# Kernel optimization log

Measured on AMD Instinct MI355X. Metric: run time of the kernel, lower is better.

## Reference

```python
import jax, jax.numpy as jnp
import numpy as np

IN_CH = 256
OUT_CH = 256
NUM_HEADS = 8
N = 4096


def setup_inputs() -> dict:
    key = jax.random.key(0)
    ks = jax.random.split(key, 12)
    s = 0.02
    return {
        "vertex_features": jax.random.normal(ks[0], (N, IN_CH), dtype=jnp.float32),
        "relative_encoding": jax.random.normal(ks[1], (N, N, NUM_HEADS), dtype=jnp.float32),
        "num_nodes": N,
        "Wq": jax.random.normal(ks[2], (IN_CH, OUT_CH), dtype=jnp.float32) * s,
        "bq": jnp.zeros((OUT_CH,), dtype=jnp.float32),
        "Wk": jax.random.normal(ks[3], (IN_CH, OUT_CH), dtype=jnp.float32) * s,
        "bk": jnp.zeros((OUT_CH,), dtype=jnp.float32),
        "Wv": jax.random.normal(ks[4], (IN_CH, OUT_CH), dtype=jnp.float32) * s,
        "bv": jnp.zeros((OUT_CH,), dtype=jnp.float32),
        "W1": jax.random.normal(ks[5], (OUT_CH // NUM_HEADS, OUT_CH), dtype=jnp.float32) * s,
        "b1": jnp.zeros((OUT_CH,), dtype=jnp.float32),
        "W2": jax.random.normal(ks[6], (OUT_CH, OUT_CH), dtype=jnp.float32) * s,
        "b2": jnp.zeros((OUT_CH,), dtype=jnp.float32),
    }


def reference(vertex_features, relative_encoding, num_nodes, Wq, bq, Wk, bk, Wv, bv, W1, b1, W2, b2):
    H = relative_encoding.shape[-1]
    # torch view(N, d, H): channel axis splits as (d, heads)
    q = (vertex_features @ Wq + bq).reshape(num_nodes, -1, H)  # [N, d, H]
    k = (vertex_features @ Wk + bk).reshape(num_nodes, -1, H)  # [N, d, H]
    v = (vertex_features @ Wv + bv).reshape(num_nodes, -1, H)  # [N, d, H]
    # q.permute(2,0,1) @ k.permute(2,1,0) -> [H,N,N], then permute(1,2,0) -> [N,N,H]
    scores = jnp.einsum('idh,jdh->ijh', q, k) + relative_encoding  # [N, N, H]
    # NOTE: softmax over the HEAD axis (dim=-1 of [N,N,H]), as in the original
    attn = jax.nn.softmax(scores, axis=-1)
    # [N,N,H] @ [N,H,d] (batched over first N) -> [N,N,d], then sum over dim=1 -> [N,d]
    attn_out = jnp.einsum('ijh,jhd->id', attn, jnp.swapaxes(v, 1, 2))  # [N, d]
    hidden = jax.nn.relu(attn_out @ W1 + b1)
    output = hidden @ W2 + b2  # [N, OUT_CH]
    return output, attn
```

## Files before the change

kernel.cpp:

```cpp
#include <hip/hip_runtime.h>

#define NN 4096
#define CH 256
#define NHEAD 8
#define DHEAD 32

typedef __attribute__((ext_vector_type(8))) short bf8_t;
typedef __attribute__((ext_vector_type(4))) float f4_t;

__device__ __forceinline__ unsigned short f2bf(float f) {
    unsigned int u = __float_as_uint(f);
    u += 0x7FFFu + ((u >> 16) & 1u);
    return (unsigned short)(u >> 16);
}

__global__ __launch_bounds__(256) void qkv_kernel(
    const float* __restrict__ X,
    const float* __restrict__ Wq, const float* __restrict__ bq,
    const float* __restrict__ Wk, const float* __restrict__ bk,
    const float* __restrict__ Wv, const float* __restrict__ bv,
    unsigned short* __restrict__ Qbf, unsigned short* __restrict__ Kbf,
    unsigned short* __restrict__ Vbf, float* __restrict__ ao)
{
    __shared__ __align__(16) float xs[16 * 256];
    const int c = threadIdx.x;
    const int i0 = blockIdx.x * 16;
    for (int r = 0; r < 16; ++r) xs[r * 256 + c] = X[(size_t)(i0 + r) * 256 + c];
    ao[(size_t)i0 * 32 + c] = 0.f;
    ao[(size_t)i0 * 32 + 256 + c] = 0.f;
    __syncthreads();

    float aq[16], ak[16], av[16];
#pragma unroll
    for (int r = 0; r < 16; ++r) { aq[r] = 0.f; ak[r] = 0.f; av[r] = 0.f; }

    for (int k = 0; k < 256; k += 4) {
        float wq0 = Wq[(k + 0) * 256 + c], wq1 = Wq[(k + 1) * 256 + c];
        float wq2 = Wq[(k + 2) * 256 + c], wq3 = Wq[(k + 3) * 256 + c];
        float wk0 = Wk[(k + 0) * 256 + c], wk1 = Wk[(k + 1) * 256 + c];
        float wk2 = Wk[(k + 2) * 256 + c], wk3 = Wk[(k + 3) * 256 + c];
        float wv0 = Wv[(k + 0) * 256 + c], wv1 = Wv[(k + 1) * 256 + c];
        float wv2 = Wv[(k + 2) * 256 + c], wv3 = Wv[(k + 3) * 256 + c];
#pragma unroll
        for (int r = 0; r < 16; ++r) {
            const float4 x = *(const float4*)&xs[r * 256 + k];
            aq[r] += x.x * wq0 + x.y * wq1 + x.z * wq2 + x.w * wq3;
            ak[r] += x.x * wk0 + x.y * wk1 + x.z * wk2 + x.w * wk3;
            av[r] += x.x * wv0 + x.y * wv1 + x.z * wv2 + x.w * wv3;
        }
    }

    const int cs = (c & 7) * 32 + (c >> 3);
    const float bqv = bq[c], bkv = bk[c], bvv = bv[c];
#pragma unroll
    for (int r = 0; r < 16; ++r) {
        const size_t row = (size_t)(i0 + r) * 256;
        Qbf[row + cs] = f2bf(aq[r] + bqv);
        Kbf[row + cs] = f2bf(ak[r] + bkv);
        Vbf[row + c]  = f2bf(av[r] + bvv);
    }
}

__global__ __launch_bounds__(256) void attn_kernel(
    const unsigned short* __restrict__ Qbf, const unsigned short* __restrict__ Kbf,
    const unsigned short* __restrict__ Vbf, const float* __restrict__ rel,
    float* __restrict__ attn_g, float* __restrict__ ao)
{
    __shared__ __align__(16) float sc_s[2048];
    __shared__ __align__(16) unsigned short at_s[16 * 136];

    const int tid = threadIdx.x;
    const int w = tid >> 6, lane = tid & 63;
    const int quad = lane >> 4, l16 = lane & 15;
    const int i0 = blockIdx.x * 16;
    const int jbase = blockIdx.y * 1024;

    bf8_t qf[2];
#pragma unroll
    for (int e = 0; e < 2; ++e) {
        const int h = 2 * w + e;
        qf[e] = *(const bf8_t*)(Qbf + (size_t)(i0 + l16) * 256 + h * 32 + quad * 8);
    }

    f4_t pv0 = {0.f, 0.f, 0.f, 0.f};
    f4_t pv1 = {0.f, 0.f, 0.f, 0.f};

    const int so  = tid * 8;
    const int sri = so >> 7, src = so & 127;
    const int jlw = w * 4 + quad;
    const int smi = tid >> 4, smj = tid & 15;

    for (int jc = 0; jc < 64; ++jc) {
        const int jb = jbase + jc * 16;

        {
            const float* gp = rel + (size_t)(i0 + sri) * 32768 + (size_t)jb * 8 + src;
            const float4 v0 = *(const float4*)gp;
            const float4 v1 = *(const float4*)(gp + 4);
            *(float4*)&sc_s[so]     = v0;
            *(float4*)&sc_s[so + 4] = v1;
        }
        __syncthreads();

#pragma unroll
        for (int e = 0; e < 2; ++e) {
            const int h = 2 * w + e;
            const bf8_t kf = *(const bf8_t*)(Kbf + (size_t)(jb + l16) * 256 + h * 32 + quad * 8);
            f4_t cf;
#pragma unroll
            for (int r = 0; r < 4; ++r) cf[r] = sc_s[(quad * 4 + r) * 128 + l16 * 8 + h];
            const f4_t d = __builtin_amdgcn_mfma_f32_16x16x32_bf16(qf[e], kf, cf, 0, 0, 0);
#pragma unroll
            for (int r = 0; r < 4; ++r) sc_s[(quad * 4 + r) * 128 + l16 * 8 + h] = d[r];
        }
        __syncthreads();

        {
            const float* sp = &sc_s[smi * 128 + smj * 8];
            const float4 s0 = *(const float4*)sp;
            const float4 s1 = *(const float4*)(sp + 4);
            float e0 = __expf(s0.x), e1 = __expf(s0.y), e2 = __expf(s0.z), e3 = __expf(s0.w);
            float e4 = __expf(s1.x), e5 = __expf(s1.y), e6 = __expf(s1.z), e7 = __expf(s1.w);
            const float inv = 1.0f / (e0 + e1 + e2 + e3 + e4 + e5 + e6 + e7);
            e0 *= inv; e1 *= inv; e2 *= inv; e3 *= inv;
            e4 *= inv; e5 *= inv; e6 *= inv; e7 *= inv;
            float* gp = attn_g + ((size_t)(i0 + smi) * 4096 + (size_t)(jb + smj)) * 8;
            *(float4*)gp       = make_float4(e0, e1, e2, e3);
            *(float4*)(gp + 4) = make_float4(e4, e5, e6, e7);
            const unsigned int p0 = (unsigned int)f2bf(e0) | ((unsigned int)f2bf(e1) << 16);
            const unsigned int p1 = (unsigned int)f2bf(e2) | ((unsigned int)f2bf(e3) << 16);
            const unsigned int p2 = (unsigned int)f2bf(e4) | ((unsigned int)f2bf(e5) << 16);
            const unsigned int p3 = (unsigned int)f2bf(e6) | ((unsigned int)f2bf(e7) << 16);
            *(uint4*)&at_s[smi * 136 + smj * 8] = make_uint4(p0, p1, p2, p3);
        }
        __syncthreads();

        {
            const bf8_t af = *(const bf8_t*)&at_s[l16 * 136 + jlw * 8];
            const unsigned short* vb = Vbf + (size_t)(jb + jlw) * 256;
            const bf8_t v0 = *(const bf8_t*)(vb + l16 * 8);
            const bf8_t v1 = *(const bf8_t*)(vb + 128 + l16 * 8);
            pv0 = __builtin_amdgcn_mfma_f32_16x16x32_bf16(af, v0, pv0, 0, 0, 0);
            pv1 = __builtin_amdgcn_mfma_f32_16x16x32_bf16(af, v1, pv1, 0, 0, 0);
        }
    }

#pragma unroll
    for (int r = 0; r < 4; ++r) {
        const size_t row = (size_t)(i0 + quad * 4 + r) * 32;
        atomicAdd(&ao[row + l16], pv0[r]);
        atomicAdd(&ao[row + 16 + l16], pv1[r]);
    }
}

__global__ __launch_bounds__(256) void mlp_kernel(
    const float* __restrict__ ao, const float* __restrict__ W1, const float* __restrict__ b1,
    const float* __restrict__ W2, const float* __restrict__ b2, float* __restrict__ out)
{
    __shared__ __align__(16) float aos[16 * 32];
    __shared__ __align__(16) float hid[16 * 256];
    const int c = threadIdx.x;
    const int i0 = blockIdx.x * 16;
    aos[c]       = ao[(size_t)i0 * 32 + c];
    aos[c + 256] = ao[(size_t)i0 * 32 + 256 + c];
    __syncthreads();

    float w1r[32];
#pragma unroll
    for (int d = 0; d < 32; ++d) w1r[d] = W1[d * 256 + c];
    const float b1v = b1[c];
    for (int r = 0; r < 16; ++r) {
        float h = b1v;
#pragma unroll
        for (int d = 0; d < 32; ++d) h += aos[r * 32 + d] * w1r[d];
        hid[r * 256 + c] = fmaxf(h, 0.f);
    }
    __syncthreads();

    float acc[16];
    const float b2v = b2[c];
#pragma unroll
    for (int r = 0; r < 16; ++r) acc[r] = b2v;
    for (int k = 0; k < 256; k += 4) {
        const float w20 = W2[(k + 0) * 256 + c], w21 = W2[(k + 1) * 256 + c];
        const float w22 = W2[(k + 2) * 256 + c], w23 = W2[(k + 3) * 256 + c];
#pragma unroll
        for (int r = 0; r < 16; ++r) {
            const float4 hh = *(const float4*)&hid[r * 256 + k];
            acc[r] += hh.x * w20 + hh.y * w21 + hh.z * w22 + hh.w * w23;
        }
    }
#pragma unroll
    for (int r = 0; r < 16; ++r) out[(size_t)(i0 + r) * 256 + c] = acc[r];
}

extern "C" void kernel_launch(void* const* d_in, const int* in_sizes, int n_in,
                              void* d_out, int out_size, void* d_ws, size_t ws_size,
                              hipStream_t stream)
{
    const float* X   = (const float*)d_in[0];
    const float* rel = (const float*)d_in[1];
    const float* Wq  = (const float*)d_in[3];
    const float* bq  = (const float*)d_in[4];
    const float* Wk  = (const float*)d_in[5];
    const float* bk  = (const float*)d_in[6];
    const float* Wv  = (const float*)d_in[7];
    const float* bv  = (const float*)d_in[8];
    const float* W1  = (const float*)d_in[9];
    const float* b1  = (const float*)d_in[10];
    const float* W2  = (const float*)d_in[11];
    const float* b2  = (const float*)d_in[12];

    float* out    = (float*)d_out;
    float* attn_g = out + (size_t)NN * CH;

    unsigned short* Qbf = (unsigned short*)d_ws;
    unsigned short* Kbf = Qbf + (size_t)NN * CH;
    unsigned short* Vbf = Kbf + (size_t)NN * CH;
    float* ao = (float*)(Vbf + (size_t)NN * CH);

    qkv_kernel<<<dim3(256), dim3(256), 0, stream>>>(X, Wq, bq, Wk, bk, Wv, bv, Qbf, Kbf, Vbf, ao);
    attn_kernel<<<dim3(256, 4), dim3(256), 0, stream>>>(Qbf, Kbf, Vbf, rel, attn_g, ao);
    mlp_kernel<<<dim3(256), dim3(256), 0, stream>>>(ao, W1, b1, W2, b2, out);
}
```

Baseline: 1.067 ms.

## Give each wave its own j-slice with all heads, dropping block barriers

The attention kernel now splits the j-range across the four waves, and each wave computes all eight heads for its 16-column tile. The relative encoding is read straight into registers, prefetched one tile ahead, and added after the MFMA, so the shared score staging buffer and every __syncthreads are gone. Softmax probabilities go to global memory with nontemporal stores, and bf16 copies go to a per-wave LDS buffer read back for the PV MFMAs. The aim is to remove barrier stalls and LDS round-trips and to overlap the large rel/attn streams with compute, at the cost of more registers (eight Q fragments, eight score accumulators, V tiles).

```diff
diff --git a/kernel.cpp b/kernel.cpp
--- a/kernel.cpp
+++ b/kernel.cpp
@@ -4,6 +4,7 @@
 #define CH 256
 #define NHEAD 8
 #define DHEAD 32
+#define RS 136
 
 typedef __attribute__((ext_vector_type(8))) short bf8_t;
 typedef __attribute__((ext_vector_type(4))) float f4_t;
@@ -66,82 +67,95 @@
     const unsigned short* __restrict__ Vbf, const float* __restrict__ rel,
     float* __restrict__ attn_g, float* __restrict__ ao)
 {
-    __shared__ __align__(16) float sc_s[2048];
-    __shared__ __align__(16) unsigned short at_s[16 * 136];
+    __shared__ __align__(16) unsigned short at_s[4][16 * RS];
 
     const int tid = threadIdx.x;
     const int w = tid >> 6, lane = tid & 63;
     const int quad = lane >> 4, l16 = lane & 15;
     const int i0 = blockIdx.x * 16;
-    const int jbase = blockIdx.y * 1024;
-
-    bf8_t qf[2];
-#pragma unroll
-    for (int e = 0; e < 2; ++e) {
-        const int h = 2 * w + e;
-        qf[e] = *(const bf8_t*)(Qbf + (size_t)(i0 + l16) * 256 + h * 32 + quad * 8);
-    }
+    const int jw0 = blockIdx.y * 1024 + w * 256;
+
+    bf8_t qf[8];
+#pragma unroll
+    for (int h = 0; h < 8; ++h)
+        qf[h] = *(const bf8_t*)(Qbf + (size_t)(i0 + l16) * 256 + h * 32 + quad * 8);
 
     f4_t pv0 = {0.f, 0.f, 0.f, 0.f};
     f4_t pv1 = {0.f, 0.f, 0.f, 0.f};
-
-    const int so  = tid * 8;
-    const int sri = so >> 7, src = so & 127;
-    const int jlw = w * 4 + quad;
-    const int smi = tid >> 4, smj = tid & 15;
-
-    for (int jc = 0; jc < 64; ++jc) {
-        const int jb = jbase + jc * 16;
-
-        {
-            const float* gp = rel + (size_t)(i0 + sri) * 32768 + (size_t)jb * 8 + src;
-            const float4 v0 = *(const float4*)gp;
-            const float4 v1 = *(const float4*)(gp + 4);
-            *(float4*)&sc_s[so]     = v0;
-            *(float4*)&sc_s[so + 4] = v1;
-        }
-        __syncthreads();
-
-#pragma unroll
-        for (int e = 0; e < 2; ++e) {
-            const int h = 2 * w + e;
-            const bf8_t kf = *(const bf8_t*)(Kbf + (size_t)(jb + l16) * 256 + h * 32 + quad * 8);
-            f4_t cf;
-#pragma unroll
-            for (int r = 0; r < 4; ++r) cf[r] = sc_s[(quad * 4 + r) * 128 + l16 * 8 + h];
-            const f4_t d = __builtin_amdgcn_mfma_f32_16x16x32_bf16(qf[e], kf, cf, 0, 0, 0);
-#pragma unroll
-            for (int r = 0; r < 4; ++r) sc_s[(quad * 4 + r) * 128 + l16 * 8 + h] = d[r];
-        }
-        __syncthreads();
-
-        {
-            const float* sp = &sc_s[smi * 128 + smj * 8];
-            const float4 s0 = *(const float4*)sp;
-            const float4 s1 = *(const float4*)(sp + 4);
-            float e0 = __expf(s0.x), e1 = __expf(s0.y), e2 = __expf(s0.z), e3 = __expf(s0.w);
-            float e4 = __expf(s1.x), e5 = __expf(s1.y), e6 = __expf(s1.z), e7 = __expf(s1.w);
+    unsigned short* ats = at_s[w];
+
+    const float* relb = rel + (size_t)(i0 + quad * 4) * (NN * 8) + (size_t)l16 * 8;
+
+    f4_t rga[4], rgb[4];
+#pragma unroll
+    for (int r = 0; r < 4; ++r) {
+        const float* gp = relb + (size_t)r * (NN * 8) + (size_t)jw0 * 8;
+        rga[r] = *(const f4_t*)gp;
+        rgb[r] = *((const f4_t*)gp + 1);
+    }
+
+    for (int t = 0; t < 16; ++t) {
+        const int jb = jw0 + t * 16;
+
+        const unsigned short* kb = Kbf + (size_t)(jb + l16) * 256 + quad * 8;
+        const f4_t z4 = {0.f, 0.f, 0.f, 0.f};
+        f4_t d[8];
+#pragma unroll
+        for (int h = 0; h < 8; ++h) {
+            const bf8_t kf = *(const bf8_t*)(kb + h * 32);
+            d[h] = __builtin_amdgcn_mfma_f32_16x16x32_bf16(qf[h], kf, z4, 0, 0, 0);
+        }
+
+        bf8_t v0s[4], v1s[4];
+        const unsigned short* vb = Vbf + (size_t)jb * 256;
+#pragma unroll
+        for (int s = 0; s < 4; ++s) {
+            const unsigned short* vp = vb + (size_t)(s * 4 + quad) * 256 + l16 * 8;
+            v0s[s] = *(const bf8_t*)vp;
+            v1s[s] = *(const bf8_t*)(vp + 128);
+        }
+
+#pragma unroll
+        for (int r = 0; r < 4; ++r) {
+            float e0 = __expf(d[0][r] + rga[r].x);
+            float e1 = __expf(d[1][r] + rga[r].y);
+            float e2 = __expf(d[2][r] + rga[r].z);
+            float e3 = __expf(d[3][r] + rga[r].w);
+            float e4 = __expf(d[4][r] + rgb[r].x);
+            float e5 = __expf(d[5][r] + rgb[r].y);
+            float e6 = __expf(d[6][r] + rgb[r].z);
+            float e7 = __expf(d[7][r] + rgb[r].w);
             const float inv = 1.0f / (e0 + e1 + e2 + e3 + e4 + e5 + e6 + e7);
             e0 *= inv; e1 *= inv; e2 *= inv; e3 *= inv;
             e4 *= inv; e5 *= inv; e6 *= inv; e7 *= inv;
-            float* gp = attn_g + ((size_t)(i0 + smi) * 4096 + (size_t)(jb + smj)) * 8;
-            *(float4*)gp       = make_float4(e0, e1, e2, e3);
-            *(float4*)(gp + 4) = make_float4(e4, e5, e6, e7);
+            float* gp = attn_g + ((size_t)(i0 + quad * 4 + r) * NN + (size_t)(jb + l16)) * 8;
+            const f4_t o0 = {e0, e1, e2, e3};
+            const f4_t o1 = {e4, e5, e6, e7};
+            __builtin_nontemporal_store(o0, (f4_t*)gp);
+            __builtin_nontemporal_store(o1, (f4_t*)gp + 1);
             const unsigned int p0 = (unsigned int)f2bf(e0) | ((unsigned int)f2bf(e1) << 16);
             const unsigned int p1 = (unsigned int)f2bf(e2) | ((unsigned int)f2bf(e3) << 16);
             const unsigned int p2 = (unsigned int)f2bf(e4) | ((unsigned int)f2bf(e5) << 16);
             const unsigned int p3 = (unsigned int)f2bf(e6) | ((unsigned int)f2bf(e7) << 16);
-            *(uint4*)&at_s[smi * 136 + smj * 8] = make_uint4(p0, p1, p2, p3);
-        }
-        __syncthreads();
-
-        {
-            const bf8_t af = *(const bf8_t*)&at_s[l16 * 136 + jlw * 8];
-            const unsigned short* vb = Vbf + (size_t)(jb + jlw) * 256;
-            const bf8_t v0 = *(const bf8_t*)(vb + l16 * 8);
-            const bf8_t v1 = *(const bf8_t*)(vb + 128 + l16 * 8);
-            pv0 = __builtin_amdgcn_mfma_f32_16x16x32_bf16(af, v0, pv0, 0, 0, 0);
-            pv1 = __builtin_amdgcn_mfma_f32_16x16x32_bf16(af, v1, pv1, 0, 0, 0);
+            *(uint4*)&ats[(quad * 4 + r) * RS + l16 * 8] = make_uint4(p0, p1, p2, p3);
+        }
+
+        if (t != 15) {
+#pragma unroll
+            for (int r = 0; r < 4; ++r) {
+                const float* gp = relb + (size_t)r * (NN * 8) + (size_t)(jb + 16) * 8;
+                rga[r] = *(const f4_t*)gp;
+                rgb[r] = *((const f4_t*)gp + 1);
+            }
+        }
+
+        asm volatile("s_waitcnt lgkmcnt(0)" ::: "memory");
+
+#pragma unroll
+        for (int s = 0; s < 4; ++s) {
+            const bf8_t af = *(const bf8_t*)&ats[l16 * RS + (s * 4 + quad) * 8];
+            pv0 = __builtin_amdgcn_mfma_f32_16x16x32_bf16(af, v0s[s], pv0, 0, 0, 0);
+            pv1 = __builtin_amdgcn_mfma_f32_16x16x32_bf16(af, v1s[s], pv1, 0, 0, 0);
         }
     }
 
```

New measurement: 1.215 ms. +13.9%, slower.

## Software-pipeline rel/K/V loads in attention kernel and double the j-split

Applied to the files above, without the earlier changes.

The attention kernel now prefetches the relative-encoding tile two chunks ahead in registers, and prefetches K and V fragments one chunk ahead, so global loads overlap the MFMA and softmax work. Barriers become explicit lgkmcnt waits plus s_barrier. The score tile in shared memory is padded to a 132-float stride to reduce bank conflicts. The j-range per block is halved to 512 with a grid of 256x8 for more parallelism, which doubles the atomic adds into the output accumulator and raises register pressure.

```diff
diff --git a/kernel.cpp b/kernel.cpp
--- a/kernel.cpp
+++ b/kernel.cpp
@@ -4,6 +4,9 @@
 #define CH 256
 #define NHEAD 8
 #define DHEAD 32
+#define RS 136
+#define SCS 132
+#define NCH 32
 
 typedef __attribute__((ext_vector_type(8))) short bf8_t;
 typedef __attribute__((ext_vector_type(4))) float f4_t;
@@ -13,6 +16,12 @@
     u += 0x7FFFu + ((u >> 16) & 1u);
     return (unsigned short)(u >> 16);
 }
+
+#define BARRIER() do {                                          \
+    asm volatile("s_waitcnt lgkmcnt(0)" ::: "memory");          \
+    __builtin_amdgcn_s_barrier();                               \
+    __builtin_amdgcn_sched_barrier(0);                          \
+} while (0)
 
 __global__ __launch_bounds__(256) void qkv_kernel(
     const float* __restrict__ X,
@@ -66,84 +75,103 @@
     const unsigned short* __restrict__ Vbf, const float* __restrict__ rel,
     float* __restrict__ attn_g, float* __restrict__ ao)
 {
-    __shared__ __align__(16) float sc_s[2048];
-    __shared__ __align__(16) unsigned short at_s[16 * 136];
+    __shared__ __align__(16) float sc_s[16 * SCS];
+    __shared__ __align__(16) unsigned short at_s[16 * RS];
 
     const int tid = threadIdx.x;
     const int w = tid >> 6, lane = tid & 63;
     const int quad = lane >> 4, l16 = lane & 15;
     const int i0 = blockIdx.x * 16;
-    const int jbase = blockIdx.y * 1024;
-
-    bf8_t qf[2];
-#pragma unroll
-    for (int e = 0; e < 2; ++e) {
-        const int h = 2 * w + e;
-        qf[e] = *(const bf8_t*)(Qbf + (size_t)(i0 + l16) * 256 + h * 32 + quad * 8);
-    }
+    const int jbase = blockIdx.y * (NCH * 16);
+
+    bf8_t qf0 = *(const bf8_t*)(Qbf + (size_t)(i0 + l16) * 256 + (2 * w + 0) * 32 + quad * 8);
+    bf8_t qf1 = *(const bf8_t*)(Qbf + (size_t)(i0 + l16) * 256 + (2 * w + 1) * 32 + quad * 8);
 
     f4_t pv0 = {0.f, 0.f, 0.f, 0.f};
     f4_t pv1 = {0.f, 0.f, 0.f, 0.f};
 
-    const int so  = tid * 8;
-    const int sri = so >> 7, src = so & 127;
+    const int so = tid * 8, sri = so >> 7, src = so & 127;
     const int jlw = w * 4 + quad;
     const int smi = tid >> 4, smj = tid & 15;
 
-    for (int jc = 0; jc < 64; ++jc) {
-        const int jb = jbase + jc * 16;
-
-        {
-            const float* gp = rel + (size_t)(i0 + sri) * 32768 + (size_t)jb * 8 + src;
-            const float4 v0 = *(const float4*)gp;
-            const float4 v1 = *(const float4*)(gp + 4);
-            *(float4*)&sc_s[so]     = v0;
-            *(float4*)&sc_s[so + 4] = v1;
-        }
-        __syncthreads();
-
-#pragma unroll
-        for (int e = 0; e < 2; ++e) {
-            const int h = 2 * w + e;
-            const bf8_t kf = *(const bf8_t*)(Kbf + (size_t)(jb + l16) * 256 + h * 32 + quad * 8);
-            f4_t cf;
-#pragma unroll
-            for (int r = 0; r < 4; ++r) cf[r] = sc_s[(quad * 4 + r) * 128 + l16 * 8 + h];
-            const f4_t d = __builtin_amdgcn_mfma_f32_16x16x32_bf16(qf[e], kf, cf, 0, 0, 0);
-#pragma unroll
-            for (int r = 0; r < 4; ++r) sc_s[(quad * 4 + r) * 128 + l16 * 8 + h] = d[r];
-        }
-        __syncthreads();
-
-        {
-            const float* sp = &sc_s[smi * 128 + smj * 8];
-            const float4 s0 = *(const float4*)sp;
-            const float4 s1 = *(const float4*)(sp + 4);
-            float e0 = __expf(s0.x), e1 = __expf(s0.y), e2 = __expf(s0.z), e3 = __expf(s0.w);
-            float e4 = __expf(s1.x), e5 = __expf(s1.y), e6 = __expf(s1.z), e7 = __expf(s1.w);
-            const float inv = 1.0f / (e0 + e1 + e2 + e3 + e4 + e5 + e6 + e7);
-            e0 *= inv; e1 *= inv; e2 *= inv; e3 *= inv;
-            e4 *= inv; e5 *= inv; e6 *= inv; e7 *= inv;
-            float* gp = attn_g + ((size_t)(i0 + smi) * 4096 + (size_t)(jb + smj)) * 8;
-            *(float4*)gp       = make_float4(e0, e1, e2, e3);
-            *(float4*)(gp + 4) = make_float4(e4, e5, e6, e7);
-            const unsigned int p0 = (unsigned int)f2bf(e0) | ((unsigned int)f2bf(e1) << 16);
-            const unsigned int p1 = (unsigned int)f2bf(e2) | ((unsigned int)f2bf(e3) << 16);
-            const unsigned int p2 = (unsigned int)f2bf(e4) | ((unsigned int)f2bf(e5) << 16);
-            const unsigned int p3 = (unsigned int)f2bf(e6) | ((unsigned int)f2bf(e7) << 16);
-            *(uint4*)&at_s[smi * 136 + smj * 8] = make_uint4(p0, p1, p2, p3);
-        }
-        __syncthreads();
-
-        {
-            const bf8_t af = *(const bf8_t*)&at_s[l16 * 136 + jlw * 8];
-            const unsigned short* vb = Vbf + (size_t)(jb + jlw) * 256;
-            const bf8_t v0 = *(const bf8_t*)(vb + l16 * 8);
-            const bf8_t v1 = *(const bf8_t*)(vb + 128 + l16 * 8);
-            pv0 = __builtin_amdgcn_mfma_f32_16x16x32_bf16(af, v0, pv0, 0, 0, 0);
-            pv1 = __builtin_amdgcn_mfma_f32_16x16x32_bf16(af, v1, pv1, 0, 0, 0);
-        }
-    }
+    const float* relp = rel + (size_t)(i0 + sri) * (NN * 8) + src;
+
+    f4_t ra0, rb0, ra1, rb1;
+    { const float* g = relp + (size_t)(jbase +  0) * 8; ra0 = *(const f4_t*)g; rb0 = *((const f4_t*)g + 1); }
+    { const float* g = relp + (size_t)(jbase + 16) * 8; ra1 = *(const f4_t*)g; rb1 = *((const f4_t*)g + 1); }
+    bf8_t kf0 = *(const bf8_t*)(Kbf + (size_t)(jbase + l16) * 256 + (2 * w + 0) * 32 + quad * 8);
+    bf8_t kf1 = *(const bf8_t*)(Kbf + (size_t)(jbase + l16) * 256 + (2 * w + 1) * 32 + quad * 8);
+
+#define CHUNK(JC, RA, RB) {                                                                     \
+    const int jb = jbase + (JC) * 16;                                                           \
+                              \
+    const unsigned short* vb = Vbf + (size_t)(jb + jlw) * 256 + l16 * 8;                        \
+    const bf8_t v0f = *(const bf8_t*)vb;                                                        \
+    const bf8_t v1f = *(const bf8_t*)(vb + 128);                                                \
+            \
+    *(f4_t*)&sc_s[sri * SCS + src]     = RA;                                                    \
+    *(f4_t*)&sc_s[sri * SCS + src + 4] = RB;                                                    \
+                                                \
+    if ((JC) + 2 < NCH) {                                                                       \
+        const float* g = relp + (size_t)(jb + 32) * 8;                                          \
+        RA = *(const f4_t*)g; RB = *((const f4_t*)g + 1);                                       \
+    }                                                                                           \
+    BARRIER();                                                                                  \
+                 \
+    {                                                                                           \
+        f4_t cf0, cf1;                                                                          \
+        _Pragma("unroll")                                                                       \
+        for (int r = 0; r < 4; ++r) cf0[r] = sc_s[(quad * 4 + r) * SCS + l16 * 8 + 2 * w];      \
+        _Pragma("unroll")                                                                       \
+        for (int r = 0; r < 4; ++r) cf1[r] = sc_s[(quad * 4 + r) * SCS + l16 * 8 + 2 * w + 1];  \
+        const f4_t d0 = __builtin_amdgcn_mfma_f32_16x16x32_bf16(qf0, kf0, cf0, 0, 0, 0);        \
+        const f4_t d1 = __builtin_amdgcn_mfma_f32_16x16x32_bf16(qf1, kf1, cf1, 0, 0, 0);        \
+        _Pragma("unroll")                                                                       \
+        for (int r = 0; r < 4; ++r) sc_s[(quad * 4 + r) * SCS + l16 * 8 + 2 * w] = d0[r];       \
+        _Pragma("unroll")                                                                       \
+        for (int r = 0; r < 4; ++r) sc_s[(quad * 4 + r) * SCS + l16 * 8 + 2 * w + 1] = d1[r];   \
+    }                                                                                           \
+    BARRIER();                                                                                  \
+            \
+    if ((JC) + 1 < NCH) {                                                                       \
+        kf0 = *(const bf8_t*)(Kbf + (size_t)(jb + 16 + l16) * 256 + (2 * w + 0) * 32 + quad * 8); \
+        kf1 = *(const bf8_t*)(Kbf + (size_t)(jb + 16 + l16) * 256 + (2 * w + 1) * 32 + quad * 8); \
+    }                                                                                           \
+                                      \
+    {                                                                                           \
+        const float* sp = &sc_s[smi * SCS + smj * 8];                                           \
+        const f4_t s0 = *(const f4_t*)sp;                                                       \
+        const f4_t s1 = *((const f4_t*)sp + 1);                                                 \
+        float e0 = __expf(s0[0]), e1 = __expf(s0[1]), e2 = __expf(s0[2]), e3 = __expf(s0[3]);   \
+        float e4 = __expf(s1[0]), e5 = __expf(s1[1]), e6 = __expf(s1[2]), e7 = __expf(s1[3]);   \
+        const float inv = 1.0f / (e0 + e1 + e2 + e3 + e4 + e5 + e6 + e7);                       \
+        e0 *= inv; e1 *= inv; e2 *= inv; e3 *= inv;                                             \
+        e4 *= inv; e5 *= inv; e6 *= inv; e7 *= inv;                                             \
+        float* gp = attn_g + ((size_t)(i0 + smi) * NN + (size_t)(jb + smj)) * 8;                \
+        const f4_t o0 = {e0, e1, e2, e3};                                                       \
+        const f4_t o1 = {e4, e5, e6, e7};                                                       \
+        *(f4_t*)gp       = o0;                                                                  \
+        *((f4_t*)gp + 1) = o1;                                                                  \
+        const unsigned int p0 = (unsigned int)f2bf(e0) | ((unsigned int)f2bf(e1) << 16);        \
+        const unsigned int p1 = (unsigned int)f2bf(e2) | ((unsigned int)f2bf(e3) << 16);        \
+        const unsigned int p2 = (unsigned int)f2bf(e4) | ((unsigned int)f2bf(e5) << 16);        \
+        const unsigned int p3 = (unsigned int)f2bf(e6) | ((unsigned int)f2bf(e7) << 16);        \
+        *(uint4*)&at_s[smi * RS + smj * 8] = make_uint4(p0, p1, p2, p3);                        \
+    }                                                                                           \
+    BARRIER();                                                                                  \
+                  \
+    {                                                                                           \
+        const bf8_t af = *(const bf8_t*)&at_s[l16 * RS + jlw * 8];                              \
+        pv0 = __builtin_amdgcn_mfma_f32_16x16x32_bf16(af, v0f, pv0, 0, 0, 0);                   \
+        pv1 = __builtin_amdgcn_mfma_f32_16x16x32_bf16(af, v1f, pv1, 0, 0, 0);                   \
+    }                                                                                           \
+}
+
+    for (int jc = 0; jc < NCH; jc += 2) {
+        CHUNK(jc,     ra0, rb0);
+        CHUNK(jc + 1, ra1, rb1);
+    }
+#undef CHUNK
 
 #pragma unroll
     for (int r = 0; r < 4; ++r) {
@@ -220,6 +248,6 @@
     float* ao = (float*)(Vbf + (size_t)NN * CH);
 
     qkv_kernel<<<dim3(256), dim3(256), 0, stream>>>(X, Wq, bq, Wk, bk, Wv, bv, Qbf, Kbf, Vbf, ao);
-    attn_kernel<<<dim3(256, 4), dim3(256), 0, stream>>>(Qbf, Kbf, Vbf, rel, attn_g, ao);
+    attn_kernel<<<dim3(256, 8), dim3(256), 0, stream>>>(Qbf, Kbf, Vbf, rel, attn_g, ao);
     mlp_kernel<<<dim3(256), dim3(256), 0, stream>>>(ao, W1, b1, W2, b2, out);
 }
```

After: 1.051 ms. About the same (-1.5%).
